# Performance work log

Measured on AMD Instinct MI355X. Metric: run time of the kernel, lower is better.

Reference implementation:

```python
import jax, jax.numpy as jnp
import numpy as np


def _conv1x1(x, w, b):
    # x: [B, C, H, W], w: [O, C], b: [O] -> [B, O, H, W]
    return jnp.einsum('bchw,oc->bohw', x, w) + b[None, :, None, None]


def _channel_branch(rgb, z, qw, qb, kw, kb, vw, vb):
    # DANet-style channel attention with reversed softmax.
    # Quirk preserved from original: q/k convs output C//8 channels, but are
    # reshaped to (B, C, H*W//8), mixing channel and spatial dims.
    B, C, H, W = rgb.shape
    q = _conv1x1(rgb, qw, qb).reshape(B, C, -1)          # [B, C, HW/8]
    k = _conv1x1(rgb, kw, kb).reshape(B, C, -1)          # [B, C, HW/8]
    energy = jnp.einsum('bcm,bdm->bcd', q, k)            # [B, C, C]
    energy_new = jnp.max(energy, axis=-1, keepdims=True) - energy
    attn = jax.nn.softmax(energy_new, axis=-1)           # [B, C, C]
    v = _conv1x1(z, vw, vb).reshape(B, C, -1)            # [B, C, HW]
    out = jnp.einsum('bcd,bdn->bcn', attn, v)            # [B, C, HW]
    return out.reshape(B, C, H, W)


def setup_inputs() -> dict:
    key = jax.random.key(0)
    ks = jax.random.split(key, 16)
    B, C = 32, 256
    Cq = C // 8
    t_h = t_w = 32
    s_h = s_w = 64
    sc = 1.0 / np.sqrt(C)
    inp = {
        'rgb_t_map': jax.random.normal(ks[0], (B, C, t_h, t_w), jnp.float32),
        'rgb_s_map': jax.random.normal(ks[1], (B, C, s_h, s_w), jnp.float32),
        'z_t_map':   jax.random.normal(ks[2], (B, C, t_h, t_w), jnp.float32),
        'z_s_map':   jax.random.normal(ks[3], (B, C, s_h, s_w), jnp.float32),
        'tq_w': jax.random.normal(ks[4], (Cq, C), jnp.float32) * sc,
        'tq_b': jnp.zeros((Cq,), jnp.float32),
        'tk_w': jax.random.normal(ks[5], (Cq, C), jnp.float32) * sc,
        'tk_b': jnp.zeros((Cq,), jnp.float32),
        'tv_w': jax.random.normal(ks[6], (C, C), jnp.float32) * sc,
        'tv_b': jnp.zeros((C,), jnp.float32),
        'sq_w': jax.random.normal(ks[7], (Cq, C), jnp.float32) * sc,
        'sq_b': jnp.zeros((Cq,), jnp.float32),
        'sk_w': jax.random.normal(ks[8], (Cq, C), jnp.float32) * sc,
        'sk_b': jnp.zeros((Cq,), jnp.float32),
        'sv_w': jax.random.normal(ks[9], (C, C), jnp.float32) * sc,
        'sv_b': jnp.zeros((C,), jnp.float32),
        'alpha': jnp.full((1,), 0.1, jnp.float32),  # nn.Parameter init is 0; nonzero for a useful baseline
        'beta':  jnp.full((1,), 0.1, jnp.float32),
    }
    return inp


def reference(rgb_t_map, rgb_s_map, z_t_map, z_s_map,
              tq_w, tq_b, tk_w, tk_b, tv_w, tv_b,
              sq_w, sq_b, sk_w, sk_b, sv_w, sv_b,
              alpha, beta):
    t_out = alpha * _channel_branch(rgb_t_map, z_t_map, tq_w, tq_b, tk_w, tk_b, tv_w, tv_b) + z_t_map
    s_out = beta * _channel_branch(rgb_s_map, z_s_map, sq_w, sq_b, sk_w, sk_b, sv_w, sv_b) + z_s_map
    return (t_out, s_out)
```

## Files before the change

kernel.cpp:

```cpp
#include <hip/hip_runtime.h>

#define HW_T 1024
#define HW_S 4096

typedef __attribute__((ext_vector_type(8))) short short8v;
typedef __attribute__((ext_vector_type(4))) float f32x4;

__device__ __forceinline__ ushort f2bf(float x) {
    unsigned u = __float_as_uint(x);
    return (ushort)((u + 0x7FFF + ((u >> 16) & 1)) >> 16);
}

__global__ __launch_bounds__(256)
void wprep_kernel(const float* __restrict__ qw_t, const float* __restrict__ kw_t,
                  const float* __restrict__ qw_s, const float* __restrict__ kw_s,
                  float* __restrict__ Wc_t, float* __restrict__ Wc_s) {
    const int br = blockIdx.x;
    const float* qw = br ? qw_s : qw_t;
    const float* kw = br ? kw_s : kw_t;
    float* Wc = br ? Wc_s : Wc_t;
    const int c = threadIdx.x;
#pragma unroll 4
    for (int cq = 0; cq < 32; cq++) {
        Wc[c * 64 + cq]      = qw[cq * 256 + c];
        Wc[c * 64 + 32 + cq] = kw[cq * 256 + c];
    }
}

#define FR8(AL, AR, AV)                                       \
    AL.x = fmaf(AV, b0.x, AL.x); AL.y = fmaf(AV, b0.y, AL.y); \
    AL.z = fmaf(AV, b0.z, AL.z); AL.w = fmaf(AV, b0.w, AL.w); \
    AR.x = fmaf(AV, b1.x, AR.x); AR.y = fmaf(AV, b1.y, AR.y); \
    AR.z = fmaf(AV, b1.z, AR.z); AR.w = fmaf(AV, b1.w, AR.w);

#define QK_OUT(ACL, ACR, RI) {                                \
    const int row = (g << 4) + (RI);                          \
    const float bv = (row < 32) ? qb[row] : kb[row & 31];     \
    float* Op = ((row < 32) ? Qo : Ko)                        \
                + (size_t)(row & 31) * HW + n0 + (j << 2);    \
    float4 o0, o1;                                            \
    o0.x = ACL.x + bv; o0.y = ACL.y + bv;                     \
    o0.z = ACL.z + bv; o0.w = ACL.w + bv;                     \
    o1.x = ACR.x + bv; o1.y = ACR.y + bv;                     \
    o1.z = ACR.z + bv; o1.w = ACR.w + bv;                     \
    *(float4*)(Op) = o0;                                      \
    *(float4*)(Op + 256) = o1; }

__global__ __launch_bounds__(256)
__attribute__((amdgpu_waves_per_eu(2, 2)))
void qk_gemm(const float* __restrict__ rgb_t, const float* __restrict__ rgb_s,
             const float* __restrict__ Wc_t, const float* __restrict__ Wc_s,
             const float* __restrict__ qb_t, const float* __restrict__ kb_t,
             const float* __restrict__ qb_s, const float* __restrict__ kb_s,
             float* __restrict__ Q_t, float* __restrict__ K_t,
             float* __restrict__ Q_s, float* __restrict__ K_s) {
    const int zb = blockIdx.y, br = zb >> 5, b = zb & 31;
    const int HW = br ? HW_S : HW_T;
    const int n0 = blockIdx.x * 512;
    if (n0 >= HW) return;

    const float* rgb = (br ? rgb_s : rgb_t) + (size_t)b * 256 * HW;
    const float* Wc  = br ? Wc_s : Wc_t;
    const float* qb  = br ? qb_s : qb_t;
    const float* kb  = br ? kb_s : kb_t;

    __shared__ float4 sW4[16][16];
    __shared__ float4 sB4[16][129];

    const int tid = threadIdx.x;
    const int g = tid >> 6;
    const int j = tid & 63;

    const int wk = tid >> 4, wr = tid & 15;
    const int bk = tid >> 4, bj = tid & 15;

    const float* Wbase = Wc + (size_t)wk * 64 + wr * 4;
    const float* Bbase = rgb + (size_t)bk * HW + n0 + bj * 4;

    float4 u0{}, u1{}, u2{}, u3{}, u4{}, u5{}, u6{}, u7{};
    float4 u8{}, u9{}, u10{}, u11{}, u12{}, u13{}, u14{}, u15{};
    float4 v0{}, v1{}, v2{}, v3{}, v4{}, v5{}, v6{}, v7{};
    float4 v8{}, v9{}, v10{}, v11{}, v12{}, v13{}, v14{}, v15{};
    float4 pw, pb0, pb1, pb2, pb3, pb4, pb5, pb6, pb7;

    pw  = *(const float4*)(Wbase);
    pb0 = *(const float4*)(Bbase);
    pb1 = *(const float4*)(Bbase + 64);
    pb2 = *(const float4*)(Bbase + 128);
    pb3 = *(const float4*)(Bbase + 192);
    pb4 = *(const float4*)(Bbase + 256);
    pb5 = *(const float4*)(Bbase + 320);
    pb6 = *(const float4*)(Bbase + 384);
    pb7 = *(const float4*)(Bbase + 448);

    for (int k0 = 0; k0 < 256; k0 += 16) {
        __syncthreads();
        sW4[wk][wr] = pw;
        sB4[bk][bj]       = pb0;
        sB4[bk][bj + 16]  = pb1;
        sB4[bk][bj + 32]  = pb2;
        sB4[bk][bj + 48]  = pb3;
        sB4[bk][bj + 64]  = pb4;
        sB4[bk][bj + 80]  = pb5;
        sB4[bk][bj + 96]  = pb6;
        sB4[bk][bj + 112] = pb7;
        __syncthreads();

        if (k0 + 16 < 256) {
            const float* Wn = Wbase + (size_t)(k0 + 16) * 64;
            const float* Bn = Bbase + (size_t)(k0 + 16) * HW;
            pw  = *(const float4*)(Wn);
            pb0 = *(const float4*)(Bn);
            pb1 = *(const float4*)(Bn + 64);
            pb2 = *(const float4*)(Bn + 128);
            pb3 = *(const float4*)(Bn + 192);
            pb4 = *(const float4*)(Bn + 256);
            pb5 = *(const float4*)(Bn + 320);
            pb6 = *(const float4*)(Bn + 384);
            pb7 = *(const float4*)(Bn + 448);
        }

#pragma unroll 2
        for (int k = 0; k < 16; k++) {
            const float4 a0 = sW4[k][(g << 2) + 0];
            const float4 a1 = sW4[k][(g << 2) + 1];
            const float4 a2 = sW4[k][(g << 2) + 2];
            const float4 a3 = sW4[k][(g << 2) + 3];
            const float4 b0 = sB4[k][j];
            const float4 b1 = sB4[k][64 + j];
            FR8(u0,  v0,  a0.x) FR8(u1,  v1,  a0.y)
            FR8(u2,  v2,  a0.z) FR8(u3,  v3,  a0.w)
            FR8(u4,  v4,  a1.x) FR8(u5,  v5,  a1.y)
            FR8(u6,  v6,  a1.z) FR8(u7,  v7,  a1.w)
            FR8(u8,  v8,  a2.x) FR8(u9,  v9,  a2.y)
            FR8(u10, v10, a2.z) FR8(u11, v11, a2.w)
            FR8(u12, v12, a3.x) FR8(u13, v13, a3.y)
            FR8(u14, v14, a3.z) FR8(u15, v15, a3.w)
        }
    }

    float* Qo = (br ? Q_s : Q_t) + (size_t)b * 32 * HW;
    float* Ko = (br ? K_s : K_t) + (size_t)b * 32 * HW;
    QK_OUT(u0,  v0,  0)  QK_OUT(u1,  v1,  1)
    QK_OUT(u2,  v2,  2)  QK_OUT(u3,  v3,  3)
    QK_OUT(u4,  v4,  4)  QK_OUT(u5,  v5,  5)
    QK_OUT(u6,  v6,  6)  QK_OUT(u7,  v7,  7)
    QK_OUT(u8,  v8,  8)  QK_OUT(u9,  v9,  9)
    QK_OUT(u10, v10, 10) QK_OUT(u11, v11, 11)
    QK_OUT(u12, v12, 12) QK_OUT(u13, v13, 13)
    QK_OUT(u14, v14, 14) QK_OUT(u15, v15, 15)
}

__global__ __launch_bounds__(256)
void attn_kernel(const float* __restrict__ Q_t, const float* __restrict__ K_t,
                 const float* __restrict__ Q_s, const float* __restrict__ K_s,
                 float* __restrict__ A_t, float* __restrict__ A_s) {
    const int zb = blockIdx.y, br = zb >> 5, b = zb & 31;
    const int M = br ? (HW_S / 8) : (HW_T / 8);
    const float* Qb = (br ? Q_s : Q_t) + (size_t)b * 32 * (br ? HW_S : HW_T);
    const float* Kb = (br ? K_s : K_t) + (size_t)b * 32 * (br ? HW_S : HW_T);
    float* attn = (br ? A_s : A_t) + (size_t)b * 65536;
    const int c0 = blockIdx.x * 32;

    __shared__ float sK[256][33];
    __shared__ float sQ[32][33];
    __shared__ float eT[32][260];

    const int tid = threadIdx.x;
    const int dx = tid & 31, cy = tid >> 5;
    float acc[4][8] = {};

    for (int m0 = 0; m0 < M; m0 += 32) {
        __syncthreads();
        {
            const int rr = tid >> 3;
            const int cc = (tid & 7) << 2;
#pragma unroll
            for (int p = 0; p < 8; p++) {
                const int row = (p << 5) + rr;
                const float4 v = *(const float4*)(Kb + (size_t)row * M + m0 + cc);
                sK[row][cc] = v.x; sK[row][cc + 1] = v.y;
                sK[row][cc + 2] = v.z; sK[row][cc + 3] = v.w;
            }
            const float4 qv = *(const float4*)(Qb + (size_t)(c0 + rr) * M + m0 + cc);
            sQ[rr][cc] = qv.x; sQ[rr][cc + 1] = qv.y;
            sQ[rr][cc + 2] = qv.z; sQ[rr][cc + 3] = qv.w;
        }
        __syncthreads();
#pragma unroll 2
        for (int m = 0; m < 32; m++) {
            float kv[8];
#pragma unroll
            for (int j = 0; j < 8; j++) kv[j] = sK[dx + (j << 5)][m];
#pragma unroll
            for (int i = 0; i < 4; i++) {
                const float qv = sQ[(cy << 2) + i][m];
#pragma unroll
                for (int j = 0; j < 8; j++) acc[i][j] = fmaf(qv, kv[j], acc[i][j]);
            }
        }
    }

#pragma unroll
    for (int i = 0; i < 4; i++)
#pragma unroll
        for (int j = 0; j < 8; j++)
            eT[(cy << 2) + i][dx + (j << 5)] = acc[i][j];
    __syncthreads();

    const int r = tid >> 3, s8 = tid & 7;
    float p[32];
    float mn = 3.0e38f;
#pragma unroll
    for (int m = 0; m < 32; m++) { p[m] = eT[r][s8 + (m << 3)]; mn = fminf(mn, p[m]); }
    mn = fminf(mn, __shfl_xor(mn, 1));
    mn = fminf(mn, __shfl_xor(mn, 2));
    mn = fminf(mn, __shfl_xor(mn, 4));
    float sum = 0.f;
#pragma unroll
    for (int m = 0; m < 32; m++) { p[m] = __expf(mn - p[m]); sum += p[m]; }
    sum += __shfl_xor(sum, 1);
    sum += __shfl_xor(sum, 2);
    sum += __shfl_xor(sum, 4);
    const float rinv = 1.0f / sum;
#pragma unroll
    for (int m = 0; m < 32; m++) eT[r][s8 + (m << 3)] = p[m] * rinv;
    __syncthreads();

    for (int idx = tid; idx < 2048; idx += 256) {
        const int row = idx >> 6, c4 = (idx & 63) << 2;
        const float4 v = *(const float4*)&eT[row][c4];
        *(float4*)(attn + (size_t)(c0 + row) * 256 + c4) = v;
    }
}

#define STA(P, OFF)                                           \
    sAf[(aslot * 4 + 0) * 260 + ar + (OFF)] = P.x;            \
    sAf[(aslot * 4 + 1) * 260 + ar + (OFF)] = P.y;            \
    sAf[(aslot * 4 + 2) * 260 + ar + (OFF)] = P.z;            \
    sAf[(aslot * 4 + 3) * 260 + ar + (OFF)] = P.w;

#define EPI_STO(AL, AR, CROW) {                               \
    const int c = (CROW);                                     \
    const size_t off0 = (size_t)c * 256 + n0 + (tx << 2);     \
    ushort4 h0, h1;                                           \
    h0.x = f2bf(AL.x); h0.y = f2bf(AL.y);                     \
    h0.z = f2bf(AL.z); h0.w = f2bf(AL.w);                     \
    h1.x = f2bf(AR.x); h1.y = f2bf(AR.y);                     \
    h1.z = f2bf(AR.z); h1.w = f2bf(AR.w);                     \
    *(ushort4*)(Co + off0) = h0;                              \
    *(ushort4*)(Co + off0 + 64) = h1; }

__global__ __launch_bounds__(256)
__attribute__((amdgpu_waves_per_eu(2, 2)))
void wgemm(const float* __restrict__ A_t, const float* __restrict__ A_s,
           const float* __restrict__ B_t, const float* __restrict__ B_s,
           ushort* __restrict__ W_t, ushort* __restrict__ W_s) {
    const int zb = blockIdx.z, br = zb >> 5, b = zb & 31;
    const int N = 256;
    const int n0 = blockIdx.x * 128;
    const float* A = (br ? A_s : A_t) + (size_t)b * 65536;
    const float* Bm = (br ? B_s : B_t);

    __shared__ float4 sA4[32][65];
    __shared__ float4 sB4[32][33];
    float* sAf = (float*)sA4;

    const int tid = threadIdx.x;
    const int tx = tid & 15, ty = tid >> 4;

    const int ar = tid >> 3, aslot = tid & 7;
    const int brow = tid >> 5, bcol = tid & 31;

    const float* Abase = A + (size_t)ar * 256 + aslot * 4;
    const float* Bbase = Bm + (size_t)brow * N + n0 + bcol * 4;

    float4 cL0{}, cL1{}, cL2{}, cL3{}, cL4{}, cL5{}, cL6{}, cL7{};
    float4 cL8{}, cL9{}, cL10{}, cL11{}, cL12{}, cL13{}, cL14{}, cL15{};
    float4 cR0{}, cR1{}, cR2{}, cR3{}, cR4{}, cR5{}, cR6{}, cR7{};
    float4 cR8{}, cR9{}, cR10{}, cR11{}, cR12{}, cR13{}, cR14{}, cR15{};
    float4 pa0, pa1, pa2, pa3, pa4, pa5, pa6, pa7, pb0, pb1, pb2, pb3;

    pa0 = *(const float4*)(Abase);
    pa1 = *(const float4*)(Abase + 8192);
    pa2 = *(const float4*)(Abase + 16384);
    pa3 = *(const float4*)(Abase + 24576);
    pa4 = *(const float4*)(Abase + 32768);
    pa5 = *(const float4*)(Abase + 40960);
    pa6 = *(const float4*)(Abase + 49152);
    pa7 = *(const float4*)(Abase + 57344);
    pb0 = *(const float4*)(Bbase);
    pb1 = *(const float4*)(Bbase + (size_t)8 * N);
    pb2 = *(const float4*)(Bbase + (size_t)16 * N);
    pb3 = *(const float4*)(Bbase + (size_t)24 * N);

    for (int k0 = 0; k0 < 256; k0 += 32) {
        __syncthreads();
        STA(pa0, 0)   STA(pa1, 32)  STA(pa2, 64)  STA(pa3, 96)
        STA(pa4, 128) STA(pa5, 160) STA(pa6, 192) STA(pa7, 224)
        sB4[brow][bcol]      = pb0;
        sB4[brow + 8][bcol]  = pb1;
        sB4[brow + 16][bcol] = pb2;
        sB4[brow + 24][bcol] = pb3;
        __syncthreads();

        if (k0 + 32 < 256) {
            const int kn = k0 + 32;
            pa0 = *(const float4*)(Abase + kn);
            pa1 = *(const float4*)(Abase + 8192 + kn);
            pa2 = *(const float4*)(Abase + 16384 + kn);
            pa3 = *(const float4*)(Abase + 24576 + kn);
            pa4 = *(const float4*)(Abase + 32768 + kn);
            pa5 = *(const float4*)(Abase + 40960 + kn);
            pa6 = *(const float4*)(Abase + 49152 + kn);
            pa7 = *(const float4*)(Abase + 57344 + kn);
            pb0 = *(const float4*)(Bbase + (size_t)kn * N);
            pb1 = *(const float4*)(Bbase + (size_t)(kn + 8) * N);
            pb2 = *(const float4*)(Bbase + (size_t)(kn + 16) * N);
            pb3 = *(const float4*)(Bbase + (size_t)(kn + 24) * N);
        }

#pragma unroll 4
        for (int k = 0; k < 32; k++) {
            const float4 a0 = sA4[k][ty];
            const float4 a1 = sA4[k][16 + ty];
            const float4 a2 = sA4[k][32 + ty];
            const float4 a3 = sA4[k][48 + ty];
            const float4 b0 = sB4[k][tx];
            const float4 b1 = sB4[k][16 + tx];
            FR8(cL0,  cR0,  a0.x) FR8(cL1,  cR1,  a0.y)
            FR8(cL2,  cR2,  a0.z) FR8(cL3,  cR3,  a0.w)
            FR8(cL4,  cR4,  a1.x) FR8(cL5,  cR5,  a1.y)
            FR8(cL6,  cR6,  a1.z) FR8(cL7,  cR7,  a1.w)
            FR8(cL8,  cR8,  a2.x) FR8(cL9,  cR9,  a2.y)
            FR8(cL10, cR10, a2.z) FR8(cL11, cR11, a2.w)
            FR8(cL12, cR12, a3.x) FR8(cL13, cR13, a3.y)
            FR8(cL14, cR14, a3.z) FR8(cL15, cR15, a3.w)
        }
    }

    ushort* Co = (br ? W_s : W_t) + (size_t)b * 65536;
    EPI_STO(cL0,  cR0,  (ty << 2) + 0)
    EPI_STO(cL1,  cR1,  (ty << 2) + 1)
    EPI_STO(cL2,  cR2,  (ty << 2) + 2)
    EPI_STO(cL3,  cR3,  (ty << 2) + 3)
    EPI_STO(cL4,  cR4,  64 + (ty << 2) + 0)
    EPI_STO(cL5,  cR5,  64 + (ty << 2) + 1)
    EPI_STO(cL6,  cR6,  64 + (ty << 2) + 2)
    EPI_STO(cL7,  cR7,  64 + (ty << 2) + 3)
    EPI_STO(cL8,  cR8,  128 + (ty << 2) + 0)
    EPI_STO(cL9,  cR9,  128 + (ty << 2) + 1)
    EPI_STO(cL10, cR10, 128 + (ty << 2) + 2)
    EPI_STO(cL11, cR11, 128 + (ty << 2) + 3)
    EPI_STO(cL12, cR12, 192 + (ty << 2) + 0)
    EPI_STO(cL13, cR13, 192 + (ty << 2) + 1)
    EPI_STO(cL14, cR14, 192 + (ty << 2) + 2)
    EPI_STO(cL15, cR15, 192 + (ty << 2) + 3)
}

__global__ __launch_bounds__(256)
void bprime_kernel(const float* __restrict__ A_t, const float* __restrict__ A_s,
                   const float* __restrict__ vb_t, const float* __restrict__ vb_s,
                   float* __restrict__ bp_t, float* __restrict__ bp_s) {
    const int bx = blockIdx.x, br = bx >> 5, b = bx & 31;
    const float* A = (br ? A_s : A_t) + (size_t)b * 65536;
    const float* vb = br ? vb_s : vb_t;
    float* bp = (br ? bp_s : bp_t) + b * 256;
    __shared__ float svb[256];
    svb[threadIdx.x] = vb[threadIdx.x];
    __syncthreads();
    const int wave = threadIdx.x >> 6, lane = threadIdx.x & 63;
    for (int c = wave; c < 256; c += 4) {
        const float4 a = *(const float4*)(A + (size_t)c * 256 + (lane << 2));
        const int l4 = lane << 2;
        float s = a.x * svb[l4] + a.y * svb[l4 + 1] + a.z * svb[l4 + 2] + a.w * svb[l4 + 3];
#pragma unroll
        for (int off = 32; off > 0; off >>= 1) s += __shfl_down(s, off);
        if (lane == 0) bp[c] = s;
    }
}

#define MF(CC, AF, BF) CC = __builtin_amdgcn_mfma_f32_16x16x32_bf16(AF, BF, CC, 0, 0, 0);

#define EPO(CC, R, C) {                                                     \
    const int cg = (w << 6) + ((R) << 4) + (lk << 2);                       \
    const size_t nn = (size_t)(n0 + ((C) << 4) + lr);                       \
    const size_t o0 = (size_t)(cg + 0) * N + nn;                            \
    const size_t o1 = (size_t)(cg + 1) * N + nn;                            \
    const size_t o2 = (size_t)(cg + 2) * N + nn;                            \
    const size_t o3 = (size_t)(cg + 3) * N + nn;                            \
    O[o0] = fmaf(alpha, CC.x + bp[cg + 0], Z[o0]);                          \
    O[o1] = fmaf(alpha, CC.y + bp[cg + 1], Z[o1]);                          \
    O[o2] = fmaf(alpha, CC.z + bp[cg + 2], Z[o2]);                          \
    O[o3] = fmaf(alpha, CC.w + bp[cg + 3], Z[o3]); }

__global__ __launch_bounds__(256)
__attribute__((amdgpu_waves_per_eu(2, 3)))
void vz_mfma(const ushort* __restrict__ W_t, const ushort* __restrict__ W_s,
             const float* __restrict__ z_t, const float* __restrict__ z_s,
             float* __restrict__ O_t, float* __restrict__ O_s,
             const float* __restrict__ bp_t, const float* __restrict__ bp_s,
             const float* __restrict__ alpha_p, const float* __restrict__ beta_p,
             int N_t, int N_s) {
    const int zb = blockIdx.y, br = zb >> 5, b = zb & 31;
    const int N = br ? N_s : N_t;
    const int n0 = blockIdx.x * 64;
    if (n0 >= N) return;
    const ushort* Wb = (br ? W_s : W_t) + (size_t)b * 65536;
    const float* Z = (br ? z_s : z_t) + (size_t)b * 256 * (size_t)N;

    __shared__ ushort sA[256 * 40];
    __shared__ ushort sB[64 * 40];

    const int tid = threadIdx.x;
    const int w = tid >> 6, l = tid & 63;
    const int lr = l & 15, lk = l >> 4;

    const int am = tid >> 2, aks = tid & 3;
    const int zn = tid & 63, zw = tid >> 6;

    const ushort* Abase = Wb + (size_t)am * 256 + aks * 8;
    const float*  Bbase = Z + (size_t)zw * N + n0 + zn;

    f32x4 c00{}, c01{}, c02{}, c03{};
    f32x4 c10{}, c11{}, c12{}, c13{};
    f32x4 c20{}, c21{}, c22{}, c23{};
    f32x4 c30{}, c31{}, c32{}, c33{};

    uint4 qa0, qa1, qa2, qa3;
    float qz0, qz1, qz2, qz3, qz4, qz5, qz6, qz7;

    qa0 = *(const uint4*)(Abase);
    qa1 = *(const uint4*)(Abase + 16384);
    qa2 = *(const uint4*)(Abase + 32768);
    qa3 = *(const uint4*)(Abase + 49152);
    qz0 = Bbase[0];
    qz1 = Bbase[(size_t)4 * N];
    qz2 = Bbase[(size_t)8 * N];
    qz3 = Bbase[(size_t)12 * N];
    qz4 = Bbase[(size_t)16 * N];
    qz5 = Bbase[(size_t)20 * N];
    qz6 = Bbase[(size_t)24 * N];
    qz7 = Bbase[(size_t)28 * N];

    const int sa0 = am * 40 + aks * 8;
    const int sb0 = zn * 40 + zw;
    const int ra = (w * 64 + lr) * 40 + lk * 8;
    const int rb = lr * 40 + lk * 8;

    for (int k0 = 0; k0 < 256; k0 += 32) {
        __syncthreads();
        *(uint4*)&sA[sa0]            = qa0;
        *(uint4*)&sA[sa0 + 64 * 40]  = qa1;
        *(uint4*)&sA[sa0 + 128 * 40] = qa2;
        *(uint4*)&sA[sa0 + 192 * 40] = qa3;
        sB[sb0]      = f2bf(qz0);
        sB[sb0 + 4]  = f2bf(qz1);
        sB[sb0 + 8]  = f2bf(qz2);
        sB[sb0 + 12] = f2bf(qz3);
        sB[sb0 + 16] = f2bf(qz4);
        sB[sb0 + 20] = f2bf(qz5);
        sB[sb0 + 24] = f2bf(qz6);
        sB[sb0 + 28] = f2bf(qz7);
        __syncthreads();

        if (k0 + 32 < 256) {
            const int kn = k0 + 32;
            qa0 = *(const uint4*)(Abase + kn);
            qa1 = *(const uint4*)(Abase + 16384 + kn);
            qa2 = *(const uint4*)(Abase + 32768 + kn);
            qa3 = *(const uint4*)(Abase + 49152 + kn);
            const float* Bn = Bbase + (size_t)kn * N;
            qz0 = Bn[0];
            qz1 = Bn[(size_t)4 * N];
            qz2 = Bn[(size_t)8 * N];
            qz3 = Bn[(size_t)12 * N];
            qz4 = Bn[(size_t)16 * N];
            qz5 = Bn[(size_t)20 * N];
            qz6 = Bn[(size_t)24 * N];
            qz7 = Bn[(size_t)28 * N];
        }

        const short8v a0 = *(const short8v*)&sA[ra];
        const short8v a1 = *(const short8v*)&sA[ra + 16 * 40];
        const short8v a2 = *(const short8v*)&sA[ra + 32 * 40];
        const short8v a3 = *(const short8v*)&sA[ra + 48 * 40];
        const short8v b0 = *(const short8v*)&sB[rb];
        const short8v b1 = *(const short8v*)&sB[rb + 16 * 40];
        const short8v b2 = *(const short8v*)&sB[rb + 32 * 40];
        const short8v b3 = *(const short8v*)&sB[rb + 48 * 40];

        MF(c00, a0, b0) MF(c01, a0, b1) MF(c02, a0, b2) MF(c03, a0, b3)
        MF(c10, a1, b0) MF(c11, a1, b1) MF(c12, a1, b2) MF(c13, a1, b3)
        MF(c20, a2, b0) MF(c21, a2, b1) MF(c22, a2, b2) MF(c23, a2, b3)
        MF(c30, a3, b0) MF(c31, a3, b1) MF(c32, a3, b2) MF(c33, a3, b3)
    }

    const float alpha = br ? beta_p[0] : alpha_p[0];
    const float* bp = (br ? bp_s : bp_t) + b * 256;
    float* O = (br ? O_s : O_t) + (size_t)b * 256 * (size_t)N;

    EPO(c00, 0, 0) EPO(c01, 0, 1) EPO(c02, 0, 2) EPO(c03, 0, 3)
    EPO(c10, 1, 0) EPO(c11, 1, 1) EPO(c12, 1, 2) EPO(c13, 1, 3)
    EPO(c20, 2, 0) EPO(c21, 2, 1) EPO(c22, 2, 2) EPO(c23, 2, 3)
    EPO(c30, 3, 0) EPO(c31, 3, 1) EPO(c32, 3, 2) EPO(c33, 3, 3)
}

extern "C" void kernel_launch(void* const* d_in, const int* in_sizes, int n_in,
                              void* d_out, int out_size, void* d_ws, size_t ws_size,
                              hipStream_t stream) {
    const float* rgb_t = (const float*)d_in[0];
    const float* rgb_s = (const float*)d_in[1];
    const float* z_t   = (const float*)d_in[2];
    const float* z_s   = (const float*)d_in[3];
    const float* tq_w  = (const float*)d_in[4];
    const float* tq_b  = (const float*)d_in[5];
    const float* tk_w  = (const float*)d_in[6];
    const float* tk_b  = (const float*)d_in[7];
    const float* tv_w  = (const float*)d_in[8];
    const float* tv_b  = (const float*)d_in[9];
    const float* sq_w  = (const float*)d_in[10];
    const float* sq_b  = (const float*)d_in[11];
    const float* sk_w  = (const float*)d_in[12];
    const float* sk_b  = (const float*)d_in[13];
    const float* sv_w  = (const float*)d_in[14];
    const float* sv_b  = (const float*)d_in[15];
    const float* alpha = (const float*)d_in[16];
    const float* beta  = (const float*)d_in[17];

    float* ws  = (float*)d_ws;
    float* At  = ws;
    float* As_ = At + 2097152;
    float* bt  = As_ + 2097152;
    float* bs  = bt + 8192;
    float* Qt  = bs + 8192;
    float* Kt  = Qt + 1048576;
    float* Qs  = Kt + 1048576;
    float* Ks  = Qs + 4194304;
    float* Wct = Ks + 4194304;
    float* Wcs = Wct + 16384;
    ushort* Wbt = (ushort*)Qt;
    ushort* Wbs = (ushort*)Qs;

    float* out_t = (float*)d_out;
    float* out_s = out_t + (size_t)32 * 256 * HW_T;

    wprep_kernel<<<dim3(2), 256, 0, stream>>>(tq_w, tk_w, sq_w, sk_w, Wct, Wcs);

    qk_gemm<<<dim3(8, 64), 256, 0, stream>>>(
        rgb_t, rgb_s, Wct, Wcs, tq_b, tk_b, sq_b, sk_b, Qt, Kt, Qs, Ks);

    attn_kernel<<<dim3(8, 64), 256, 0, stream>>>(Qt, Kt, Qs, Ks, At, As_);

    bprime_kernel<<<dim3(64), 256, 0, stream>>>(At, As_, tv_b, sv_b, bt, bs);

    wgemm<<<dim3(2, 1, 64), 256, 0, stream>>>(At, As_, tv_w, sv_w, Wbt, Wbs);

    vz_mfma<<<dim3(64, 64), 256, 0, stream>>>(
        Wbt, Wbs, z_t, z_s, out_t, out_s, bt, bs, alpha, beta, HW_T, HW_S);
}
```

Baseline: 683.8 us.

## Load vz_mfma A operand straight to registers, pack B stores, compact grid

The A (weight) tile in vz_mfma is now loaded from global memory directly into the MFMA register fragments, so its shared-memory staging buffer and LDS traffic go away. The z tile is written to LDS as one packed 128-bit store of eight bf16 values per thread, using an XOR-swizzled layout meant to avoid bank conflicts. The grid becomes a flat 1D launch of exactly 512+2048 blocks, removing the early-exit blocks of the old 64x64 grid. The waves_per_eu attribute is also dropped. The cost is that each wave reads its A rows from global memory on its own instead of sharing them through LDS, which puts more load on the caches.

```diff
diff --git a/kernel.cpp b/kernel.cpp
--- a/kernel.cpp
+++ b/kernel.cpp
@@ -9,6 +9,9 @@
 __device__ __forceinline__ ushort f2bf(float x) {
     unsigned u = __float_as_uint(x);
     return (ushort)((u + 0x7FFF + ((u >> 16) & 1)) >> 16);
+}
+__device__ __forceinline__ unsigned pk2(float lo, float hi) {
+    return (unsigned)f2bf(lo) | ((unsigned)f2bf(hi) << 16);
 }
 
 __global__ __launch_bounds__(256)
@@ -395,100 +398,89 @@
     O[o3] = fmaf(alpha, CC.w + bp[cg + 3], Z[o3]); }
 
 __global__ __launch_bounds__(256)
-__attribute__((amdgpu_waves_per_eu(2, 3)))
 void vz_mfma(const ushort* __restrict__ W_t, const ushort* __restrict__ W_s,
              const float* __restrict__ z_t, const float* __restrict__ z_s,
              float* __restrict__ O_t, float* __restrict__ O_s,
              const float* __restrict__ bp_t, const float* __restrict__ bp_s,
              const float* __restrict__ alpha_p, const float* __restrict__ beta_p,
              int N_t, int N_s) {
-    const int zb = blockIdx.y, br = zb >> 5, b = zb & 31;
+    const int bid = blockIdx.x;
+    int br, b, nb;
+    if (bid < 512) { br = 0; b = bid >> 4; nb = bid & 15; }
+    else { const int r = bid - 512; br = 1; b = r >> 6; nb = r & 63; }
     const int N = br ? N_s : N_t;
-    const int n0 = blockIdx.x * 64;
-    if (n0 >= N) return;
+    const int n0 = nb * 64;
     const ushort* Wb = (br ? W_s : W_t) + (size_t)b * 65536;
     const float* Z = (br ? z_s : z_t) + (size_t)b * 256 * (size_t)N;
 
-    __shared__ ushort sA[256 * 40];
     __shared__ ushort sB[64 * 40];
 
     const int tid = threadIdx.x;
     const int w = tid >> 6, l = tid & 63;
     const int lr = l & 15, lk = l >> 4;
 
-    const int am = tid >> 2, aks = tid & 3;
     const int zn = tid & 63, zw = tid >> 6;
-
-    const ushort* Abase = Wb + (size_t)am * 256 + aks * 8;
-    const float*  Bbase = Z + (size_t)zw * N + n0 + zn;
+    const float* Bbase = Z + (size_t)(zw * 8) * N + n0 + zn;
+    const int sbw = zn * 40 + ((zw << 3) ^ (((zn >> 3) & 3) << 3));
+
+    const ushort* Arow = Wb + (size_t)(w * 64 + lr) * 256 + lk * 8;
+
+    const int rb0 = (0 * 16 + lr) * 40 + ((lk << 3) ^ ((((0 * 16 + lr) >> 3) & 3) << 3));
+    const int rb1 = (1 * 16 + lr) * 40 + ((lk << 3) ^ ((((1 * 16 + lr) >> 3) & 3) << 3));
+    const int rb2 = (2 * 16 + lr) * 40 + ((lk << 3) ^ ((((2 * 16 + lr) >> 3) & 3) << 3));
+    const int rb3 = (3 * 16 + lr) * 40 + ((lk << 3) ^ ((((3 * 16 + lr) >> 3) & 3) << 3));
 
     f32x4 c00{}, c01{}, c02{}, c03{};
     f32x4 c10{}, c11{}, c12{}, c13{};
     f32x4 c20{}, c21{}, c22{}, c23{};
     f32x4 c30{}, c31{}, c32{}, c33{};
 
-    uint4 qa0, qa1, qa2, qa3;
     float qz0, qz1, qz2, qz3, qz4, qz5, qz6, qz7;
-
-    qa0 = *(const uint4*)(Abase);
-    qa1 = *(const uint4*)(Abase + 16384);
-    qa2 = *(const uint4*)(Abase + 32768);
-    qa3 = *(const uint4*)(Abase + 49152);
+    short8v pa0, pa1, pa2, pa3;
+
     qz0 = Bbase[0];
-    qz1 = Bbase[(size_t)4 * N];
-    qz2 = Bbase[(size_t)8 * N];
-    qz3 = Bbase[(size_t)12 * N];
-    qz4 = Bbase[(size_t)16 * N];
-    qz5 = Bbase[(size_t)20 * N];
-    qz6 = Bbase[(size_t)24 * N];
-    qz7 = Bbase[(size_t)28 * N];
-
-    const int sa0 = am * 40 + aks * 8;
-    const int sb0 = zn * 40 + zw;
-    const int ra = (w * 64 + lr) * 40 + lk * 8;
-    const int rb = lr * 40 + lk * 8;
+    qz1 = Bbase[(size_t)1 * N];
+    qz2 = Bbase[(size_t)2 * N];
+    qz3 = Bbase[(size_t)3 * N];
+    qz4 = Bbase[(size_t)4 * N];
+    qz5 = Bbase[(size_t)5 * N];
+    qz6 = Bbase[(size_t)6 * N];
+    qz7 = Bbase[(size_t)7 * N];
+    pa0 = *(const short8v*)(Arow);
+    pa1 = *(const short8v*)(Arow + 16 * 256);
+    pa2 = *(const short8v*)(Arow + 32 * 256);
+    pa3 = *(const short8v*)(Arow + 48 * 256);
 
     for (int k0 = 0; k0 < 256; k0 += 32) {
         __syncthreads();
-        *(uint4*)&sA[sa0]            = qa0;
-        *(uint4*)&sA[sa0 + 64 * 40]  = qa1;
-        *(uint4*)&sA[sa0 + 128 * 40] = qa2;
-        *(uint4*)&sA[sa0 + 192 * 40] = qa3;
-        sB[sb0]      = f2bf(qz0);
-        sB[sb0 + 4]  = f2bf(qz1);
-        sB[sb0 + 8]  = f2bf(qz2);
-        sB[sb0 + 12] = f2bf(qz3);
-        sB[sb0 + 16] = f2bf(qz4);
-        sB[sb0 + 20] = f2bf(qz5);
-        sB[sb0 + 24] = f2bf(qz6);
-        sB[sb0 + 28] = f2bf(qz7);
-        __syncthreads();
-
+        uint4 pk;
+        pk.x = pk2(qz0, qz1); pk.y = pk2(qz2, qz3);
+        pk.z = pk2(qz4, qz5); pk.w = pk2(qz6, qz7);
+        *(uint4*)&sB[sbw] = pk;
+        __syncthreads();
+
+        const short8v a0 = pa0, a1 = pa1, a2 = pa2, a3 = pa3;
         if (k0 + 32 < 256) {
             const int kn = k0 + 32;
-            qa0 = *(const uint4*)(Abase + kn);
-            qa1 = *(const uint4*)(Abase + 16384 + kn);
-            qa2 = *(const uint4*)(Abase + 32768 + kn);
-            qa3 = *(const uint4*)(Abase + 49152 + kn);
             const float* Bn = Bbase + (size_t)kn * N;
             qz0 = Bn[0];
-            qz1 = Bn[(size_t)4 * N];
-            qz2 = Bn[(size_t)8 * N];
-            qz3 = Bn[(size_t)12 * N];
-            qz4 = Bn[(size_t)16 * N];
-            qz5 = Bn[(size_t)20 * N];
-            qz6 = Bn[(size_t)24 * N];
-            qz7 = Bn[(size_t)28 * N];
-        }
-
-        const short8v a0 = *(const short8v*)&sA[ra];
-        const short8v a1 = *(const short8v*)&sA[ra + 16 * 40];
-        const short8v a2 = *(const short8v*)&sA[ra + 32 * 40];
-        const short8v a3 = *(const short8v*)&sA[ra + 48 * 40];
-        const short8v b0 = *(const short8v*)&sB[rb];
-        const short8v b1 = *(const short8v*)&sB[rb + 16 * 40];
-        const short8v b2 = *(const short8v*)&sB[rb + 32 * 40];
-        const short8v b3 = *(const short8v*)&sB[rb + 48 * 40];
+            qz1 = Bn[(size_t)1 * N];
+            qz2 = Bn[(size_t)2 * N];
+            qz3 = Bn[(size_t)3 * N];
+            qz4 = Bn[(size_t)4 * N];
+            qz5 = Bn[(size_t)5 * N];
+            qz6 = Bn[(size_t)6 * N];
+            qz7 = Bn[(size_t)7 * N];
+            pa0 = *(const short8v*)(Arow + kn);
+            pa1 = *(const short8v*)(Arow + 16 * 256 + kn);
+            pa2 = *(const short8v*)(Arow + 32 * 256 + kn);
+            pa3 = *(const short8v*)(Arow + 48 * 256 + kn);
+        }
+
+        const short8v b0 = *(const short8v*)&sB[rb0];
+        const short8v b1 = *(const short8v*)&sB[rb1];
+        const short8v b2 = *(const short8v*)&sB[rb2];
+        const short8v b3 = *(const short8v*)&sB[rb3];
 
         MF(c00, a0, b0) MF(c01, a0, b1) MF(c02, a0, b2) MF(c03, a0, b3)
         MF(c10, a1, b0) MF(c11, a1, b1) MF(c12, a1, b2) MF(c13, a1, b3)
@@ -556,6 +548,6 @@
 
     wgemm<<<dim3(2, 1, 64), 256, 0, stream>>>(At, As_, tv_w, sv_w, Wbt, Wbs);
 
-    vz_mfma<<<dim3(64, 64), 256, 0, stream>>>(
+    vz_mfma<<<dim3(2560), 256, 0, stream>>>(
         Wbt, Wbs, z_t, z_s, out_t, out_s, bt, bs, alpha, beta, HW_T, HW_S);
 }
```

Result: faster. 669.6 us (-2.1%).
